# Kernel optimization log

Hardware: AMD Instinct MI355X
Metric: run time of the kernel (lower is better)

## Reference

```python
import jax, jax.numpy as jnp
import numpy as np

N = 50000
E = 800000
NODE_IN, EDGE_IN, HID, OUT, L = 32, 16, 128, 128, 2


def _layer_norm(h, g, b, eps=1e-5):
    mu = jnp.mean(h, axis=-1, keepdims=True)
    var = jnp.var(h, axis=-1, keepdims=True)
    return (h - mu) * jax.lax.rsqrt(var + eps) * g + b


def setup_inputs() -> dict:
    key = jax.random.key(0)
    ks = jax.random.split(key, 20)
    s = lambda k, shape, fan: jax.random.normal(k, shape, jnp.float32) * (1.0 / np.sqrt(fan))
    return {
        "x": jax.random.normal(ks[0], (N, NODE_IN), jnp.float32),
        "edge_index": jax.random.randint(ks[1], (2, E), 0, N, jnp.int64),
        "edge_attr": jax.random.normal(ks[2], (E, EDGE_IN), jnp.float32),
        "enc_W": s(ks[3], (NODE_IN, HID), NODE_IN),
        "enc_b": jnp.zeros((HID,), jnp.float32),
        "enc_g": jnp.ones((HID,), jnp.float32),
        "enc_beta": jnp.zeros((HID,), jnp.float32),
        "msg_W1": s(ks[4], (L, 2 * HID + EDGE_IN, HID), 2 * HID + EDGE_IN),
        "msg_b1": jnp.zeros((L, HID), jnp.float32),
        "msg_W2": s(ks[5], (L, HID, HID), HID),
        "msg_b2": jnp.zeros((L, HID), jnp.float32),
        "upd_W1": s(ks[6], (L, 2 * HID, HID), 2 * HID),
        "upd_b1": jnp.zeros((L, HID), jnp.float32),
        "upd_W2": s(ks[7], (L, HID, HID), HID),
        "upd_b2": jnp.zeros((L, HID), jnp.float32),
        "ln_g": jnp.ones((L, HID), jnp.float32),
        "ln_beta": jnp.zeros((L, HID), jnp.float32),
        "head_W": s(ks[8], (HID, OUT), HID),
        "head_b": jnp.zeros((OUT,), jnp.float32),
    }


def reference(x, edge_index, edge_attr, enc_W, enc_b, enc_g, enc_beta,
              msg_W1, msg_b1, msg_W2, msg_b2, upd_W1, upd_b1, upd_W2, upd_b2,
              ln_g, ln_beta, head_W, head_b):
    src = edge_index[0]  # x_j (source)
    tgt = edge_index[1]  # x_i (target, aggregation index)
    n = x.shape[0]

    # node encoder: Linear -> ReLU -> LayerNorm
    h = jax.nn.relu(x @ enc_W + enc_b)
    h = _layer_norm(h, enc_g, enc_beta)

    # per-edge incoming-degree for mean aggregation (isolated nodes -> 0)
    cnt = jax.ops.segment_sum(jnp.ones((tgt.shape[0],), h.dtype), tgt, num_segments=n)
    denom = jnp.maximum(cnt, 1.0)[:, None]

    for l in range(L):
        x_i = h[tgt]                                 # [E, HID]
        x_j = h[src]                                 # [E, HID]
        msg_in = jnp.concatenate([x_i, x_j, edge_attr], axis=-1)  # [E, 2H+Ed]
        m = jax.nn.relu(msg_in @ msg_W1[l] + msg_b1[l]) @ msg_W2[l] + msg_b2[l]
        aggr = jax.ops.segment_sum(m, tgt, num_segments=n) / denom  # mean
        upd_in = jnp.concatenate([h, aggr], axis=-1)
        out = jax.nn.relu(upd_in @ upd_W1[l] + upd_b1[l]) @ upd_W2[l] + upd_b2[l]
        h = _layer_norm(h + out, ln_g[l], ln_beta[l])

    return h @ head_W + head_b
```

## Files before the change

### kernel.cpp

```cpp
#include <hip/hip_runtime.h>
#include <hip/hip_bf16.h>
#include <stdint.h>

#define N_NODES 50000
#define N_EDGES 800000
#define NL 2

#define KS2 136
#define KSU 264

typedef __bf16 bf16x8 __attribute__((ext_vector_type(8)));
typedef float f32x4 __attribute__((ext_vector_type(4)));

__device__ __forceinline__ f32x4 mfma_bf16(uint4 a, uint4 b, f32x4 c) {
    return __builtin_amdgcn_mfma_f32_16x16x32_bf16(
        __builtin_bit_cast(bf16x8, a), __builtin_bit_cast(bf16x8, b), c, 0, 0, 0);
}

__device__ __forceinline__ unsigned short f2b(float f) {
    union { float f; unsigned u; } v; v.f = f;
    unsigned r = v.u + 0x7FFFu + ((v.u >> 16) & 1u);
    return (unsigned short)(r >> 16);
}

__device__ __forceinline__ float b2f(unsigned short u) {
    union { unsigned u; float f; } v; v.u = ((unsigned)u) << 16; return v.f;
}

template<int KSTEPS, int BSTR>
__device__ __forceinline__ void gemm8(const unsigned short* aLane,
                                      const unsigned short* bLane, f32x4 acc[8]) {
#pragma unroll
    for (int kc = 0; kc < KSTEPS; kc++) {
        uint4 a = *(const uint4*)(aLane + kc * 32);
#pragma unroll
        for (int ct = 0; ct < 8; ct++) {
            uint4 b = *(const uint4*)(bLane + (size_t)ct * 16 * BSTR + kc * 32);
            acc[ct] = mfma_bf16(a, b, acc[ct]);
        }
    }
}

template<int KSTEPS, int ASTR, int BSTR>
__device__ __forceinline__ void gemm_2x4(const unsigned short* aLane,
                                         const unsigned short* bLane,
                                         f32x4 acc[4][2]) {
#pragma unroll
    for (int kc = 0; kc < KSTEPS; kc++) {
        uint4 b0 = *(const uint4*)(bLane + kc * 32);
        uint4 b1 = *(const uint4*)(bLane + (size_t)16 * BSTR + kc * 32);
#pragma unroll
        for (int rt = 0; rt < 4; rt++) {
            uint4 a = *(const uint4*)(aLane + (size_t)rt * 16 * ASTR + kc * 32);
            acc[rt][0] = mfma_bf16(a, b0, acc[rt][0]);
            acc[rt][1] = mfma_bf16(a, b1, acc[rt][1]);
        }
    }
}

__global__ void prep_kernel(const float* __restrict__ mW1,
                            const float* __restrict__ uW1, const float* __restrict__ uW2,
                            const float* __restrict__ hW,
                            unsigned short* __restrict__ wab, unsigned short* __restrict__ w1cp,
                            unsigned short* __restrict__ u1t, unsigned short* __restrict__ u2t,
                            unsigned short* __restrict__ ht) {
    int i = blockIdx.x * 256 + threadIdx.x;
    const int SA = NL * 256 * 136;
    const int SC = NL * 128 * 32;
    const int SU = NL * 128 * KSU;
    const int S3 = NL * 128 * KS2;
    const int S4 = 128 * KS2;
    if (i < SA) {
        int l = i / (256 * 136), r = i % (256 * 136), j = r / 136, k = r % 136;
        float v = 0.f;
        if (k < 128)
            v = (j < 128) ? mW1[((size_t)l * 272 + k) * 128 + j]
                          : mW1[((size_t)l * 272 + 128 + k) * 128 + (j - 128)];
        wab[i] = f2b(v);
        return;
    }
    i -= SA;
    if (i < SC) {
        int l = i / (128 * 32), r = i % (128 * 32), j = r / 32, k = r % 32;
        w1cp[i] = (k < 16) ? f2b(mW1[((size_t)l * 272 + 256 + k) * 128 + j]) : (unsigned short)0;
        return;
    }
    i -= SC;
    if (i < SU) {
        int l = i / (128 * KSU), r = i % (128 * KSU), n = r / KSU, k = r % KSU;
        if (k < 128)       u1t[i] = f2b(uW1[((size_t)l * 256 + k) * 128 + n]);
        else if (k >= 256) u1t[i] = 0;
        return;
    }
    i -= SU;
    if (i < S3) {
        int l = i / (128 * KS2), r = i % (128 * KS2), n = r / KS2, k = r % KS2;
        u2t[i] = (k < 128) ? f2b(uW2[((size_t)l * 128 + k) * 128 + n]) : (unsigned short)0;
        return;
    }
    i -= S3;
    if (i < S4) {
        int n = i / KS2, k = i % KS2;
        ht[i] = (k < 128) ? f2b(hW[(size_t)k * 128 + n]) : (unsigned short)0;
    }
}

__global__ void prep2_kernel(const float* __restrict__ mW2, const float* __restrict__ uW1,
                             unsigned short* __restrict__ u1t) {
    __shared__ float w2row[128];
    const int l = blockIdx.x >> 7, j = blockIdx.x & 127;
    const int n = threadIdx.x;
    w2row[n] = mW2[((size_t)l * 128 + j) * 128 + n];
    __syncthreads();
    float s = 0.f;
#pragma unroll 8
    for (int c = 0; c < 128; c++)
        s += w2row[c] * uW1[((size_t)l * 256 + 128 + c) * 128 + n];
    u1t[(size_t)l * 128 * KSU + (size_t)n * KSU + 128 + j] = f2b(s);
}

__global__ void prep3_kernel(const float* __restrict__ mb2, const float* __restrict__ uW1,
                             float* __restrict__ bfold) {
    const int l = blockIdx.x;
    const int n = threadIdx.x;
    float s = 0.f;
#pragma unroll 8
    for (int c = 0; c < 128; c++)
        s += mb2[l * 128 + c] * uW1[((size_t)l * 256 + 128 + c) * 128 + n];
    bfold[l * 128 + n] = s;
}

__global__ __launch_bounds__(256) void enc_kernel(
        const float* __restrict__ x, const float* __restrict__ W,
        const float* __restrict__ b, const float* __restrict__ g, const float* __restrict__ bet,
        float* __restrict__ h, unsigned short* __restrict__ hb) {
    __shared__ float sx[64];
    __shared__ float redS[4], redSS[4];
    const int t = threadIdx.x;
    const int nb = blockIdx.x * 2;
    if (t < 64) sx[t] = x[(size_t)nb * 32 + t];
    __syncthreads();
    const int half = t >> 7, j = t & 127;
    const int node = nb + half;
    float acc = b[j];
#pragma unroll
    for (int k = 0; k < 32; k++) acc += sx[half * 32 + k] * W[k * 128 + j];
    float v = fmaxf(acc, 0.f);
    float s = v, ss = v * v;
#pragma unroll
    for (int d = 32; d > 0; d >>= 1) { s += __shfl_down(s, d); ss += __shfl_down(ss, d); }
    const int wv = t >> 6;
    if ((t & 63) == 0) { redS[wv] = s; redSS[wv] = ss; }
    __syncthreads();
    float S = redS[half * 2] + redS[half * 2 + 1];
    float SS = redSS[half * 2] + redSS[half * 2 + 1];
    float mu = S * (1.f / 128.f);
    float var = SS * (1.f / 128.f) - mu * mu;
    float rs = rsqrtf(var + 1e-5f);
    float o = (v - mu) * rs * g[j] + bet[j];
    h[(size_t)node * 128 + j] = o;
    hb[(size_t)node * 128 + j] = f2b(o);
}

__global__ void hist_kernel(const int* __restrict__ tgt, int* __restrict__ hist) {
    int i = blockIdx.x * 256 + threadIdx.x;
    atomicAdd(hist + tgt[i], 1);
}

__global__ void scan1_kernel(const int* __restrict__ hist, int* __restrict__ incl,
                             int* __restrict__ blksum) {
    __shared__ int buf[256];
    const int t = threadIdx.x;
    const int i = blockIdx.x * 256 + t;
    int v = (i < N_NODES) ? hist[i] : 0;
    buf[t] = v; __syncthreads();
#pragma unroll
    for (int d = 1; d < 256; d <<= 1) {
        int x = (t >= d) ? buf[t - d] : 0;
        __syncthreads();
        buf[t] += x;
        __syncthreads();
    }
    if (i < N_NODES) incl[i] = buf[t];
    if (t == 255) blksum[blockIdx.x] = buf[255];
}

__global__ void scan2_kernel(int* __restrict__ blksum, int nblk) {
    __shared__ int buf[256];
    const int t = threadIdx.x;
    int v = (t < nblk) ? blksum[t] : 0;
    buf[t] = v; __syncthreads();
#pragma unroll
    for (int d = 1; d < 256; d <<= 1) {
        int x = (t >= d) ? buf[t - d] : 0;
        __syncthreads();
        buf[t] += x;
        __syncthreads();
    }
    if (t < nblk) blksum[t] = buf[t];
}

__global__ void scan3_kernel(int* __restrict__ incl, const int* __restrict__ blksum,
                             const int* __restrict__ hist) {
    const int i = blockIdx.x * 256 + threadIdx.x;
    if (i >= N_NODES) return;
    const int b = blockIdx.x;
    const int base = (b > 0) ? blksum[b - 1] : 0;
    incl[i] = incl[i] + base - hist[i];
}

__global__ void scatter_kernel(const int* __restrict__ src, const int* __restrict__ tgt,
                               const float* __restrict__ ea, int* __restrict__ cursor,
                               unsigned short* __restrict__ sSrc, unsigned short* __restrict__ sTgt,
                               unsigned short* __restrict__ eabS) {
    const int e = blockIdx.x * 256 + threadIdx.x;
    const int tg = tgt[e];
    const int p = atomicAdd(cursor + tg, 1);
    sSrc[p] = (unsigned short)src[e];
    sTgt[p] = (unsigned short)tg;
    const float4* s = (const float4*)(ea + (size_t)e * 16);
    ushort4* d = (ushort4*)(eabS + (size_t)p * 16);
#pragma unroll
    for (int i = 0; i < 4; i++) {
        float4 v = s[i];
        d[i] = make_ushort4(f2b(v.x), f2b(v.y), f2b(v.z), f2b(v.w));
    }
}

__global__ __launch_bounds__(256, 4) void node_kernel(
        const unsigned short* __restrict__ hb, const unsigned short* __restrict__ wab,
        const float* __restrict__ b1,
        unsigned short* __restrict__ Tb, unsigned short* __restrict__ Sb) {
    __shared__ __align__(16) unsigned short As[64 * KS2];
    const int t = threadIdx.x;
    const int n0 = blockIdx.x * 64;
    {
        const int m = t >> 2, q = t & 3;
        const int node = n0 + m;
        uint4* dst = (uint4*)(As + m * KS2);
        if (node < N_NODES) {
            const uint4* s = (const uint4*)(hb + (size_t)node * 128);
#pragma unroll
            for (int i = 0; i < 4; i++) dst[q * 4 + i] = s[q * 4 + i];
        } else {
            uint4 z{0, 0, 0, 0};
            for (int i = q; i < 16; i += 4) dst[i] = z;
        }
    }
    __syncthreads();

    const int wv = t >> 6, lane = t & 63, lr = lane & 15, lq = lane >> 4;
    const int cb = wv * 64;
    const f32x4 z4 = {0.f, 0.f, 0.f, 0.f};
    f32x4 acc[4][4];
#pragma unroll
    for (int i = 0; i < 4; i++)
#pragma unroll
        for (int j = 0; j < 4; j++) acc[i][j] = z4;

    const unsigned short* aL = As + lr * KS2 + lq * 8;
    const unsigned short* bL = wab + (size_t)(cb + lr) * KS2 + lq * 8;
#pragma unroll
    for (int kc = 0; kc < 4; kc++) {
        uint4 bA = *(const uint4*)(bL + kc * 32);
        uint4 bB = *(const uint4*)(bL + (size_t)16 * KS2 + kc * 32);
        uint4 bC = *(const uint4*)(bL + (size_t)32 * KS2 + kc * 32);
        uint4 bD = *(const uint4*)(bL + (size_t)48 * KS2 + kc * 32);
#pragma unroll
        for (int rt = 0; rt < 4; rt++) {
            uint4 a = *(const uint4*)(aL + (size_t)rt * 16 * KS2 + kc * 32);
            acc[rt][0] = mfma_bf16(a, bA, acc[rt][0]);
            acc[rt][1] = mfma_bf16(a, bB, acc[rt][1]);
            acc[rt][2] = mfma_bf16(a, bC, acc[rt][2]);
            acc[rt][3] = mfma_bf16(a, bD, acc[rt][3]);
        }
    }
#pragma unroll
    for (int ct = 0; ct < 4; ct++) {
        const int j = cb + ct * 16 + lr;
        const float bias = (j < 128) ? b1[j] : 0.f;
#pragma unroll
        for (int rt = 0; rt < 4; rt++) {
#pragma unroll
            for (int r = 0; r < 4; r++) {
                const int node = n0 + rt * 16 + lq * 4 + r;
                if (node < N_NODES) {
                    const float v = acc[rt][ct][r] + bias;
                    if (j < 128) Tb[(size_t)node * 128 + j] = f2b(v);
                    else         Sb[(size_t)node * 128 + (j - 128)] = f2b(v);
                }
            }
        }
    }
}

__global__ __launch_bounds__(256, 4) void edge_kernel(
        const unsigned short* __restrict__ eabS,
        const unsigned short* __restrict__ sSrc, const unsigned short* __restrict__ sTgt,
        const unsigned short* __restrict__ w1cp,
        const unsigned short* __restrict__ Tb, const unsigned short* __restrict__ Sb,
        float* __restrict__ aggr) {
    __shared__ __align__(16) unsigned short Or[128 * 136];
    __shared__ int sT[128];
    __shared__ int sS[128];

    const int t = threadIdx.x;
    const int e0 = blockIdx.x * 128;
    if (t < 128) { sT[t] = sTgt[e0 + t]; sS[t] = sSrc[e0 + t]; }
    __syncthreads();

    const int wv = t >> 6, lane = t & 63, lr = lane & 15, lq = lane >> 4;
    const f32x4 z4 = {0.f, 0.f, 0.f, 0.f};
#pragma unroll
    for (int rh = 0; rh < 2; rh++) {
        const int rt = wv * 2 + rh;
        uint4 a = {0, 0, 0, 0};
        if (lq < 2) a = *(const uint4*)(eabS + (size_t)(e0 + rt * 16 + lr) * 16 + lq * 8);
        f32x4 acc[8];
#pragma unroll
        for (int ct = 0; ct < 8; ct++) {
            uint4 b = *(const uint4*)(w1cp + (ct * 16 + lr) * 32 + lq * 8);
            acc[ct] = mfma_bf16(a, b, z4);
        }
#pragma unroll
        for (int ct = 0; ct < 8; ct++) {
            const int col = ct * 16 + lr;
#pragma unroll
            for (int r = 0; r < 4; r++) {
                const int row = rt * 16 + lq * 4 + r;
                const float tv = b2f(Tb[(size_t)sT[row] * 128 + col]);
                const float sv = b2f(Sb[(size_t)sS[row] * 128 + col]);
                Or[row * 136 + col] = f2b(fmaxf(acc[ct][r] + tv + sv, 0.f));
            }
        }
    }
    __syncthreads();

    {
        const int c = t >> 1;
        const int rb = (t & 1) * 64;
        float s = 0.f;
        int cur = sT[rb];
        for (int i = 0; i < 64; i++) {
            const int rg = rb + i;
            const int tg = sT[rg];
            if (tg != cur) {
                atomicAdd(aggr + (size_t)cur * 128 + c, s);
                s = 0.f; cur = tg;
            }
            s += b2f(Or[rg * 136 + c]);
        }
        atomicAdd(aggr + (size_t)cur * 128 + c, s);
    }
}

__global__ __launch_bounds__(256, 4) void upd_kernel(
        const unsigned short* __restrict__ hb_in, const float* __restrict__ h_in,
        const float* __restrict__ aggr, const int* __restrict__ hist,
        const unsigned short* __restrict__ u1t, const unsigned short* __restrict__ u2t,
        const float* __restrict__ b1, const float* __restrict__ bf,
        const float* __restrict__ b2,
        const float* __restrict__ g, const float* __restrict__ bet,
        float* __restrict__ h_out, unsigned short* __restrict__ hb_out) {
    __shared__ __align__(16) char smemA[64 * KSU * 2];
    __shared__ float sF[64];
    unsigned short* As = (unsigned short*)smemA;
    float* LNb = (float*)smemA;

    const int t = threadIdx.x;
    const int n0 = blockIdx.x * 64;
    {
        const int m = t >> 2, q = t & 3;
        const int node = n0 + m;
        unsigned short* row = As + m * KSU;
        if (node < N_NODES) {
            const uint4* ph = (const uint4*)(hb_in + (size_t)node * 128);
            uint4* d0 = (uint4*)row;
#pragma unroll
            for (int i = 0; i < 4; i++) d0[q * 4 + i] = ph[q * 4 + i];
            const int cntv = hist[node];
            if (q == 0) sF[m] = (cntv > 0) ? 1.f : 0.f;
            const float rden = 1.0f / fmaxf((float)cntv, 1.0f);
            const float4* pa = (const float4*)(aggr + (size_t)node * 128 + q * 32);
            ushort4* d1 = (ushort4*)(row + 128 + q * 32);
#pragma unroll
            for (int i = 0; i < 8; i++) {
                float4 v = pa[i];
                d1[i] = make_ushort4(f2b(v.x * rden), f2b(v.y * rden),
                                     f2b(v.z * rden), f2b(v.w * rden));
            }
            if (q == 0) { uint4 z{0, 0, 0, 0}; ((uint4*)(row + 256))[0] = z; }
        } else {
            if (q == 0) sF[m] = 0.f;
            uint4 z{0, 0, 0, 0};
            uint4* d = (uint4*)row;
            for (int i = q; i < 33; i += 4) d[i] = z;
        }
    }
    __syncthreads();

    const int wv = t >> 6, lane = t & 63, lr = lane & 15, lq = lane >> 4;
    const int cb = wv * 32;
    const f32x4 z4 = {0.f, 0.f, 0.f, 0.f};

    f32x4 acc[4][2];
#pragma unroll
    for (int i = 0; i < 4; i++) { acc[i][0] = z4; acc[i][1] = z4; }
    gemm_2x4<8, KSU, KSU>(As + lr * KSU + lq * 8,
                          u1t + (size_t)(cb + lr) * KSU + lq * 8, acc);
    __syncthreads();

#pragma unroll
    for (int ct = 0; ct < 2; ct++) {
        const int col = cb + ct * 16 + lr;
        const float bv = b1[col];
        const float bfv = bf[col];
#pragma unroll
        for (int rt = 0; rt < 4; rt++) {
#pragma unroll
            for (int r = 0; r < 4; r++) {
                const int ml = rt * 16 + lq * 4 + r;
                float v = fmaxf(acc[rt][ct][r] + bv + sF[ml] * bfv, 0.f);
                As[ml * KSU + col] = f2b(v);
            }
        }
    }
    __syncthreads();

    f32x4 acc2[4][2];
#pragma unroll
    for (int i = 0; i < 4; i++) { acc2[i][0] = z4; acc2[i][1] = z4; }
    gemm_2x4<4, KSU, KS2>(As + lr * KSU + lq * 8,
                          u2t + (size_t)(cb + lr) * KS2 + lq * 8, acc2);
    __syncthreads();

#pragma unroll
    for (int ct = 0; ct < 2; ct++) {
        const int col = cb + ct * 16 + lr;
        const float bv = b2[col];
#pragma unroll
        for (int rt = 0; rt < 4; rt++) {
#pragma unroll
            for (int r = 0; r < 4; r++) {
                const int ml = rt * 16 + lq * 4 + r;
                const int node = n0 + ml;
                if (node < N_NODES)
                    LNb[ml * 132 + col] = acc2[rt][ct][r] + bv + h_in[(size_t)node * 128 + col];
            }
        }
    }
    __syncthreads();

    {
        const int r = t >> 2, c0 = (t & 3) * 32;
        const int node = n0 + r;
        if (node < N_NODES) {
            float s = 0.f, ss = 0.f;
#pragma unroll
            for (int i = 0; i < 32; i++) { float v = LNb[r * 132 + c0 + i]; s += v; ss += v * v; }
            s += __shfl_xor(s, 1); ss += __shfl_xor(ss, 1);
            s += __shfl_xor(s, 2); ss += __shfl_xor(ss, 2);
            const float mu = s * (1.0f / 128.0f);
            const float var = ss * (1.0f / 128.0f) - mu * mu;
            const float rs = rsqrtf(var + 1e-5f);
#pragma unroll
            for (int i = 0; i < 32; i++) {
                const int j = c0 + i;
                float v = (LNb[r * 132 + j] - mu) * rs * g[j] + bet[j];
                h_out[(size_t)node * 128 + j] = v;
                hb_out[(size_t)node * 128 + j] = f2b(v);
            }
        }
    }
}

__global__ __launch_bounds__(256, 2) void head_kernel(
        const unsigned short* __restrict__ hb, const unsigned short* __restrict__ ht,
        const float* __restrict__ hbias, float* __restrict__ out) {
    __shared__ __align__(16) unsigned short As[64 * KS2];
    const int t = threadIdx.x;
    const int n0 = blockIdx.x * 64;
    {
        const int m = t >> 2, q = t & 3;
        const int node = n0 + m;
        uint4* dst = (uint4*)(As + m * KS2);
        if (node < N_NODES) {
            const uint4* s = (const uint4*)(hb + (size_t)node * 128);
#pragma unroll
            for (int i = 0; i < 4; i++) dst[q * 4 + i] = s[q * 4 + i];
        } else {
            uint4 z{0, 0, 0, 0};
            for (int i = q; i < 16; i += 4) dst[i] = z;
        }
    }
    __syncthreads();

    const int wv = t >> 6, lane = t & 63, lr = lane & 15, lq = lane >> 4;
    const int m0 = wv * 16;
    const f32x4 z4 = {0.f, 0.f, 0.f, 0.f};
    f32x4 acc[8];
#pragma unroll
    for (int i = 0; i < 8; i++) acc[i] = z4;
    gemm8<4, KS2>(As + (m0 + lr) * KS2 + lq * 8, ht + (size_t)lr * KS2 + lq * 8, acc);
#pragma unroll
    for (int ct = 0; ct < 8; ct++) {
        const int col = ct * 16 + lr;
        const float bv = hbias[col];
#pragma unroll
        for (int r = 0; r < 4; r++) {
            const int node = n0 + m0 + lq * 4 + r;
            if (node < N_NODES) out[(size_t)node * 128 + col] = acc[ct][r] + bv;
        }
    }
}

extern "C" void kernel_launch(void* const* d_in, const int* in_sizes, int n_in,
                              void* d_out, int out_size, void* d_ws, size_t ws_size,
                              hipStream_t stream) {
    const float* x       = (const float*)d_in[0];
    const int*   ei      = (const int*)d_in[1];
    const float* ea      = (const float*)d_in[2];
    const float* encW    = (const float*)d_in[3];
    const float* encb    = (const float*)d_in[4];
    const float* encg    = (const float*)d_in[5];
    const float* encbeta = (const float*)d_in[6];
    const float* msgW1   = (const float*)d_in[7];
    const float* msgb1   = (const float*)d_in[8];
    const float* msgW2   = (const float*)d_in[9];
    const float* msgb2   = (const float*)d_in[10];
    const float* updW1   = (const float*)d_in[11];
    const float* updb1   = (const float*)d_in[12];
    const float* updW2   = (const float*)d_in[13];
    const float* updb2   = (const float*)d_in[14];
    const float* lng     = (const float*)d_in[15];
    const float* lnbeta  = (const float*)d_in[16];
    const float* headW   = (const float*)d_in[17];
    const float* headb   = (const float*)d_in[18];

    char* w = (char*)d_ws;
    size_t off = 0;
    auto nxt = [&](size_t bytes) -> void* {
        void* p = w + off;
        off = (off + bytes + 255) & ~(size_t)255;
        return p;
    };
    float*          h     = (float*)nxt((size_t)N_NODES * 128 * 4);
    unsigned short* hb    = (unsigned short*)nxt((size_t)N_NODES * 128 * 2);
    float*          aggr  = (float*)nxt((size_t)N_NODES * 128 * 4);
    unsigned short* Tb    = (unsigned short*)nxt((size_t)N_NODES * 128 * 2);
    unsigned short* Sb    = (unsigned short*)nxt((size_t)N_NODES * 128 * 2);
    unsigned short* eabS  = (unsigned short*)nxt((size_t)N_EDGES * 16 * 2);
    unsigned short* sSrc  = (unsigned short*)nxt((size_t)N_EDGES * 2);
    unsigned short* sTgtS = (unsigned short*)nxt((size_t)N_EDGES * 2);
    int*            hist  = (int*)nxt((size_t)N_NODES * 4);
    int*            incl  = (int*)nxt((size_t)N_NODES * 4);
    int*            blksum= (int*)nxt(256 * 4);
    unsigned short* wab   = (unsigned short*)nxt((size_t)NL * 256 * 136 * 2);
    unsigned short* w1cp  = (unsigned short*)nxt((size_t)NL * 128 * 32 * 2);
    unsigned short* u1t   = (unsigned short*)nxt((size_t)NL * 128 * KSU * 2);
    unsigned short* u2t   = (unsigned short*)nxt((size_t)NL * 128 * KS2 * 2);
    unsigned short* ht    = (unsigned short*)nxt((size_t)128 * KS2 * 2);
    float*          bfold = (float*)nxt((size_t)NL * 128 * 4);

    const int NBLK = (N_NODES + 255) / 256;
    const int PREP_N = NL * 256 * 136 + NL * 128 * 32 + NL * 128 * KSU
                     + NL * 128 * KS2 + 128 * KS2;

    hipMemsetAsync(hist, 0, (size_t)N_NODES * 4, stream);
    prep_kernel<<<(PREP_N + 255) / 256, 256, 0, stream>>>(msgW1, updW1, updW2, headW,
                                                          wab, w1cp, u1t, u2t, ht);
    prep2_kernel<<<NL * 128, 128, 0, stream>>>(msgW2, updW1, u1t);
    prep3_kernel<<<NL, 128, 0, stream>>>(msgb2, updW1, bfold);
    enc_kernel<<<25000, 256, 0, stream>>>(x, encW, encb, encg, encbeta, h, hb);
    hist_kernel<<<3125, 256, 0, stream>>>(ei + N_EDGES, hist);
    scan1_kernel<<<NBLK, 256, 0, stream>>>(hist, incl, blksum);
    scan2_kernel<<<1, 256, 0, stream>>>(blksum, NBLK);
    scan3_kernel<<<NBLK, 256, 0, stream>>>(incl, blksum, hist);
    scatter_kernel<<<3125, 256, 0, stream>>>(ei, ei + N_EDGES, ea, incl,
                                             sSrc, sTgtS, eabS);

    for (int l = 0; l < NL; l++) {
        node_kernel<<<782, 256, 0, stream>>>(hb, wab + (size_t)l * 256 * 136,
                                             msgb1 + l * 128, Tb, Sb);
        hipMemsetAsync(aggr, 0, (size_t)N_NODES * 128 * 4, stream);
        edge_kernel<<<6250, 256, 0, stream>>>(eabS, sSrc, sTgtS,
                                              w1cp + (size_t)l * 128 * 32,
                                              Tb, Sb, aggr);
        upd_kernel<<<782, 256, 0, stream>>>(hb, h, aggr, hist,
                                            u1t + (size_t)l * 128 * KSU,
                                            u2t + (size_t)l * 128 * KS2,
                                            updb1 + l * 128, bfold + l * 128,
                                            updb2 + l * 128,
                                            lng + l * 128, lnbeta + l * 128, h, hb);
    }
    head_kernel<<<782, 256, 0, stream>>>(hb, ht, headb, (float*)d_out);
}
```

Baseline: 583.4 us.

## Vectorize edge gathers of node rows and shrink edge tile to 64

```diff
diff --git a/kernel.cpp b/kernel.cpp
--- a/kernel.cpp
+++ b/kernel.cpp
@@ -8,6 +8,7 @@
 
 #define KS2 136
 #define KSU 264
+#define ESTR 133
 
 typedef __bf16 bf16x8 __attribute__((ext_vector_type(8)));
 typedef float f32x4 __attribute__((ext_vector_type(4)));
@@ -25,6 +26,12 @@
 
 __device__ __forceinline__ float b2f(unsigned short u) {
     union { unsigned u; float f; } v; v.u = ((unsigned)u) << 16; return v.f;
+}
+__device__ __forceinline__ float b2f_lo(unsigned u) {
+    union { unsigned u; float f; } v; v.u = u << 16; return v.f;
+}
+__device__ __forceinline__ float b2f_hi(unsigned u) {
+    union { unsigned u; float f; } v; v.u = u & 0xFFFF0000u; return v.f;
 }
 
 template<int KSTEPS, int BSTR>
@@ -300,22 +307,19 @@
         const unsigned short* __restrict__ w1cp,
         const unsigned short* __restrict__ Tb, const unsigned short* __restrict__ Sb,
         float* __restrict__ aggr) {
-    __shared__ __align__(16) unsigned short Or[128 * 136];
-    __shared__ int sT[128];
-    __shared__ int sS[128];
+    __shared__ float Es[64 * ESTR];
+    __shared__ int sT[64];
+    __shared__ int sS[64];
 
     const int t = threadIdx.x;
-    const int e0 = blockIdx.x * 128;
-    if (t < 128) { sT[t] = sTgt[e0 + t]; sS[t] = sSrc[e0 + t]; }
-    __syncthreads();
+    const int e0 = blockIdx.x * 64;
+    if (t < 64) { sT[t] = sTgt[e0 + t]; sS[t] = sSrc[e0 + t]; }
 
     const int wv = t >> 6, lane = t & 63, lr = lane & 15, lq = lane >> 4;
     const f32x4 z4 = {0.f, 0.f, 0.f, 0.f};
-#pragma unroll
-    for (int rh = 0; rh < 2; rh++) {
-        const int rt = wv * 2 + rh;
+    {
         uint4 a = {0, 0, 0, 0};
-        if (lq < 2) a = *(const uint4*)(eabS + (size_t)(e0 + rt * 16 + lr) * 16 + lq * 8);
+        if (lq < 2) a = *(const uint4*)(eabS + (size_t)(e0 + wv * 16 + lr) * 16 + lq * 8);
         f32x4 acc[8];
 #pragma unroll
         for (int ct = 0; ct < 8; ct++) {
@@ -326,29 +330,47 @@
         for (int ct = 0; ct < 8; ct++) {
             const int col = ct * 16 + lr;
 #pragma unroll
-            for (int r = 0; r < 4; r++) {
-                const int row = rt * 16 + lq * 4 + r;
-                const float tv = b2f(Tb[(size_t)sT[row] * 128 + col]);
-                const float sv = b2f(Sb[(size_t)sS[row] * 128 + col]);
-                Or[row * 136 + col] = f2b(fmaxf(acc[ct][r] + tv + sv, 0.f));
-            }
+            for (int r = 0; r < 4; r++)
+                Es[(wv * 16 + lq * 4 + r) * ESTR + col] = acc[ct][r];
+        }
+    }
+    __syncthreads();
+
+    {
+        const int m = t & 63;
+        const int c8b = t >> 6;
+        const unsigned short* Trow = Tb + (size_t)sT[m] * 128;
+        const unsigned short* Srow = Sb + (size_t)sS[m] * 128;
+        float* Erow = Es + m * ESTR;
+#pragma unroll
+        for (int it = 0; it < 4; it++) {
+            const int c0 = (c8b + it * 4) * 8;
+            const uint4 tv = *(const uint4*)(Trow + c0);
+            const uint4 sv = *(const uint4*)(Srow + c0);
+            float tf[8] = {b2f_lo(tv.x), b2f_hi(tv.x), b2f_lo(tv.y), b2f_hi(tv.y),
+                           b2f_lo(tv.z), b2f_hi(tv.z), b2f_lo(tv.w), b2f_hi(tv.w)};
+            float sf[8] = {b2f_lo(sv.x), b2f_hi(sv.x), b2f_lo(sv.y), b2f_hi(sv.y),
+                           b2f_lo(sv.z), b2f_hi(sv.z), b2f_lo(sv.w), b2f_hi(sv.w)};
+#pragma unroll
+            for (int i = 0; i < 8; i++)
+                Erow[c0 + i] = fmaxf(Erow[c0 + i] + tf[i] + sf[i], 0.f);
         }
     }
     __syncthreads();
 
     {
         const int c = t >> 1;
-        const int rb = (t & 1) * 64;
+        const int rb = (t & 1) * 32;
         float s = 0.f;
         int cur = sT[rb];
-        for (int i = 0; i < 64; i++) {
+        for (int i = 0; i < 32; i++) {
             const int rg = rb + i;
             const int tg = sT[rg];
             if (tg != cur) {
                 atomicAdd(aggr + (size_t)cur * 128 + c, s);
                 s = 0.f; cur = tg;
             }
-            s += b2f(Or[rg * 136 + c]);
+            s += Es[rg * ESTR + c];
         }
         atomicAdd(aggr + (size_t)cur * 128 + c, s);
     }
@@ -583,9 +605,9 @@
         node_kernel<<<782, 256, 0, stream>>>(hb, wab + (size_t)l * 256 * 136,
                                              msgb1 + l * 128, Tb, Sb);
         hipMemsetAsync(aggr, 0, (size_t)N_NODES * 128 * 4, stream);
-        edge_kernel<<<6250, 256, 0, stream>>>(eabS, sSrc, sTgtS,
-                                              w1cp + (size_t)l * 128 * 32,
-                                              Tb, Sb, aggr);
+        edge_kernel<<<12500, 256, 0, stream>>>(eabS, sSrc, sTgtS,
+                                               w1cp + (size_t)l * 128 * 32,
+                                               Tb, Sb, aggr);
         upd_kernel<<<782, 256, 0, stream>>>(hb, h, aggr, hist,
                                             u1t + (size_t)l * 128 * KSU,
                                             u2t + (size_t)l * 128 * KS2,
```

Result: no change. 576.7 us (-1.2%).
